# Optimization experiments

Measured on AMD Instinct MI355X. Metric: run time of the kernel, lower is better.

Reference implementation:

```python
import jax, jax.numpy as jnp
import numpy as np

NF, B, C, H, W = 5, 8, 64, 128, 128

def setup_inputs() -> dict:
    key = jax.random.key(0)
    k1, k2, k3, k4, k5 = jax.random.split(key, 5)
    return {
        "inp": jax.random.normal(k1, (NF, B, C, H, W), dtype=jnp.float32),
        "origin_w": jax.random.normal(k2, (C, NF * C), dtype=jnp.float32) * 0.05,
        "origin_b": jax.random.normal(k3, (C,), dtype=jnp.float32) * 0.05,
        "out_w": jax.random.normal(k4, (1, 2 * C), dtype=jnp.float32) * 0.05,
        "out_b": jax.random.normal(k5, (1,), dtype=jnp.float32) * 0.05,
    }

def reference(inp, origin_w, origin_b, out_w, out_b):
    nf, b, c, h, w = inp.shape
    # concat frames along channel dim: [b, nf*c, h, w]
    x = jnp.transpose(inp, (1, 0, 2, 3, 4)).reshape(b, nf * c, h, w)
    # 1x1 conv -> origin query, viewed as [b, c, 1, h*w]
    origin = jnp.einsum('ok,bkhw->bohw', origin_w, x) + origin_b[None, :, None, None]
    origin = origin.reshape(b, c, 1, h * w)
    last = inp[-1]  # [b, c, h, w]
    # difference basis: [b, c, nf-1, h*w]
    basis = jnp.stack([last - inp[i] for i in range(nf - 1)], axis=2).reshape(b, c, nf - 1, h * w)
    # L2 normalize over the spatial (last) dim, torch F.normalize semantics (eps=1e-12)
    norm = jnp.sqrt(jnp.sum(basis * basis, axis=-1, keepdims=True))
    basis1 = basis / jnp.maximum(norm, 1e-12)
    # tiny-MN batched matmuls: [b,c,1,hw] x [b,c,hw,nf-1] -> [b,c,1,nf-1]
    score = jnp.einsum('bcik,bcjk->bcij', origin, basis1)
    # [b,c,1,nf-1] x [b,c,nf-1,hw] -> [b,c,1,hw]; original views back as (b,c,w,h)
    out = jnp.einsum('bcij,bcjk->bcik', score, basis1).reshape(b, c, w, h)
    cat = jnp.concatenate([out, last], axis=1)  # [b, 2c, h, w]
    y = jnp.einsum('ok,bkhw->bohw', out_w, cat) + out_b[None, :, None, None]
    return y
```

## Files before the change

kernel.cpp:

```cpp
#include <hip/hip_runtime.h>
#include <math.h>

#define NF 5
#define NB 8
#define NC 64
#define HW 16384
#define NK 320
#define FSTRIDE (NB*NC*HW)

#define EN_FLOATS    (NB*NC*8)
#define ALPHA_FLOATS (NB*NK)

__global__ void k0_wp(const float* __restrict__ W, float* __restrict__ Wp){
    int idx = blockIdx.x*256 + threadIdx.x;
    if (idx < NC*NK){
        int c = idx / NK;
        int k = idx - c*NK;
        Wp[((c>>3)*NK + k)*8 + (c&7)] = W[idx];
    }
}

__device__ __forceinline__ float redsum64(float v){
#pragma unroll
    for (int m = 1; m < 64; m <<= 1) v += __shfl_xor(v, m, 64);
    return v;
}

__global__ __launch_bounds__(512, 4) void k1_fused(
    const float* __restrict__ inp, const float* __restrict__ Wp,
    const float* __restrict__ bias, float* __restrict__ EN)
{
    const int tid = threadIdx.x;
    const int l   = tid & 63;
    const int wv  = __builtin_amdgcn_readfirstlane(tid >> 6);
    const int c0  = wv << 3;
    const int b   = blockIdx.x >> 6;
    const int s0  = (blockIdx.x & 63) << 8;

    float4 a0,a1,a2,a3,a4,a5,a6,a7;
    {
        float4 b0 = *reinterpret_cast<const float4*>(bias + c0);
        float4 b1 = *reinterpret_cast<const float4*>(bias + c0 + 4);
        a0 = make_float4(b0.x,b0.x,b0.x,b0.x);
        a1 = make_float4(b0.y,b0.y,b0.y,b0.y);
        a2 = make_float4(b0.z,b0.z,b0.z,b0.z);
        a3 = make_float4(b0.w,b0.w,b0.w,b0.w);
        a4 = make_float4(b1.x,b1.x,b1.x,b1.x);
        a5 = make_float4(b1.y,b1.y,b1.y,b1.y);
        a6 = make_float4(b1.z,b1.z,b1.z,b1.z);
        a7 = make_float4(b1.w,b1.w,b1.w,b1.w);
    }

    const float* wbase = Wp + (size_t)wv * (NK*8);

#define FMA4(A, WS) \
    A.x = fmaf(WS, xv.x, A.x); A.y = fmaf(WS, xv.y, A.y); \
    A.z = fmaf(WS, xv.z, A.z); A.w = fmaf(WS, xv.w, A.w);

#pragma unroll 1
    for (int f=0; f<NF; ++f){
        const float* xp = inp + (size_t)(f*NB + b)*NC*HW + s0 + (l << 2);
        const float* wf = wbase + f*64*8;
#pragma unroll 8
        for (int k=0; k<64; ++k){
            float4 xv = *reinterpret_cast<const float4*>(xp);
            xp += HW;
            const float* wk = wf + (k << 3);
            float4 w0 = *reinterpret_cast<const float4*>(wk);
            float4 w1 = *reinterpret_cast<const float4*>(wk + 4);
            FMA4(a0, w0.x) FMA4(a1, w0.y) FMA4(a2, w0.z) FMA4(a3, w0.w)
            FMA4(a4, w1.x) FMA4(a5, w1.y) FMA4(a6, w1.z) FMA4(a7, w1.w)
        }
    }
#undef FMA4

#define PHASEB(CC, ACC) { \
    const float* cb = inp + ((size_t)b*NC + (c0+(CC)))*HW + s0 + (l << 2); \
    float4 x4 = *reinterpret_cast<const float4*>(cb + (size_t)4*FSTRIDE); \
    float ev[4], nv[4]; \
    _Pragma("unroll") \
    for (int i=0; i<4; ++i){ \
        float4 xi = *reinterpret_cast<const float4*>(cb + (size_t)i*FSTRIDE); \
        float dx = x4.x - xi.x, dy = x4.y - xi.y; \
        float dz = x4.z - xi.z, dw = x4.w - xi.w; \
        nv[i] = fmaf(dx,dx, fmaf(dy,dy, fmaf(dz,dz, dw*dw))); \
        ev[i] = fmaf((ACC).x,dx, fmaf((ACC).y,dy, fmaf((ACC).z,dz, (ACC).w*dw))); \
    } \
    _Pragma("unroll") \
    for (int i=0; i<4; ++i){ ev[i] = redsum64(ev[i]); nv[i] = redsum64(nv[i]); } \
    if (l == 0){ \
        float* p = EN + ((size_t)b*NC + c0 + (CC))*8; \
        atomicAdd(p+0, ev[0]); atomicAdd(p+1, ev[1]); \
        atomicAdd(p+2, ev[2]); atomicAdd(p+3, ev[3]); \
        atomicAdd(p+4, nv[0]); atomicAdd(p+5, nv[1]); \
        atomicAdd(p+6, nv[2]); atomicAdd(p+7, nv[3]); \
    } }

    PHASEB(0, a0) PHASEB(1, a1) PHASEB(2, a2) PHASEB(3, a3)
    PHASEB(4, a4) PHASEB(5, a5) PHASEB(6, a6) PHASEB(7, a7)
#undef PHASEB
}

__global__ void k2_coef(const float* __restrict__ EN, const float* __restrict__ out_w,
                        float* __restrict__ alpha)
{
    int tid = threadIdx.x;
    int b = tid >> 6, c = tid & 63;
    const float* e = EN + (b*NC + c)*8;
    float w1 = out_w[c], w2 = out_w[NC + c];
    float csum = 0.f;
#pragma unroll
    for (int i=0; i<4; ++i){
        float nc = fmaxf(sqrtf(e[4+i]), 1e-12f);
        float coef = e[i] / (nc*nc);
        alpha[b*NK + i*NC + c] = -w1*coef;
        csum += coef;
    }
    alpha[b*NK + 4*NC + c] = w1*csum + w2;
}

__global__ __launch_bounds__(512, 4) void k3_out(const float* __restrict__ inp,
        const float* __restrict__ alpha, const float* __restrict__ out_b,
        float* __restrict__ y)
{
    __shared__ float4 P[512];
    const int tid = threadIdx.x;
    const int b   = blockIdx.x >> 6;
    const int s0  = (blockIdx.x & 63) << 8;
    const int sg  = tid & 63;
    const int rg  = __builtin_amdgcn_readfirstlane(tid >> 6);

    float4 acc = make_float4(0.f, 0.f, 0.f, 0.f);
    const float* abase = alpha + b*NK + rg*40;
#pragma unroll 8
    for (int j=0; j<40; ++j){
        int r = rg*40 + j;
        const float* p = inp + (size_t)(((r>>6)*NB + b)*NC + (r&63))*HW + s0 + (sg<<2);
        float  w  = abase[j];
        float4 xv = *reinterpret_cast<const float4*>(p);
        acc.x = fmaf(w, xv.x, acc.x); acc.y = fmaf(w, xv.y, acc.y);
        acc.z = fmaf(w, xv.z, acc.z); acc.w = fmaf(w, xv.w, acc.w);
    }
    P[tid] = acc;
    __syncthreads();
    if (tid < 64){
        float4 r0 = P[tid];
        float vx = r0.x, vy = r0.y, vz = r0.z, vw = r0.w;
#pragma unroll
        for (int g=1; g<8; ++g){
            float4 q = P[tid + (g<<6)];
            vx += q.x; vy += q.y; vz += q.z; vw += q.w;
        }
        float bb = out_b[0];
        float4 o = make_float4(vx+bb, vy+bb, vz+bb, vw+bb);
        *reinterpret_cast<float4*>(y + (size_t)b*HW + s0 + (tid<<2)) = o;
    }
}

extern "C" void kernel_launch(void* const* d_in, const int* in_sizes, int n_in,
                              void* d_out, int out_size, void* d_ws, size_t ws_size,
                              hipStream_t stream)
{
    const float* inp      = (const float*)d_in[0];
    const float* origin_w = (const float*)d_in[1];
    const float* origin_b = (const float*)d_in[2];
    const float* out_w    = (const float*)d_in[3];
    const float* out_b    = (const float*)d_in[4];
    float* y  = (float*)d_out;
    float* ws = (float*)d_ws;

    float* EN    = ws;
    float* alpha = ws + EN_FLOATS;
    float* Wp    = ws + EN_FLOATS + ALPHA_FLOATS;

    hipMemsetAsync(EN, 0, EN_FLOATS*sizeof(float), stream);
    k0_wp   <<<(NC*NK + 255)/256, 256, 0, stream>>>(origin_w, Wp);
    k1_fused<<<512, 512, 0, stream>>>(inp, Wp, origin_b, EN);
    k2_coef <<<1, NB*NC, 0, stream>>>(EN, out_w, alpha);
    k3_out  <<<512, 512, 0, stream>>>(inp, alpha, out_b, y);
}
```

Baseline: 330.0 us.

## Split k1 into 4-channel waves with XCD-aware mapping and fold coef kernel into k3

Reworks k1 so that each wave accumulates 4 output channels instead of 8, with 2048 blocks of 256 threads. Block indices are remapped so that the four channel-group blocks sharing a spatial tile land on the same XCD, which lets them share the input reads in L2. The memset is merged into the weight-repack kernel and the k2 coefficient kernel is folded into k3 through shared memory, removing two launches. The cost is that each input element is now read by four blocks instead of one, which leans on L2 hits, and k3 recomputes the coefficients in every block.

After: 353.5 us. +7.1%, slower.

```diff
diff --git a/kernel.cpp b/kernel.cpp
--- a/kernel.cpp
+++ b/kernel.cpp
@@ -9,15 +9,21 @@
 #define FSTRIDE (NB*NC*HW)
 
 #define EN_FLOATS    (NB*NC*8)
-#define ALPHA_FLOATS (NB*NK)
 
-__global__ void k0_wp(const float* __restrict__ W, float* __restrict__ Wp){
-    int idx = blockIdx.x*256 + threadIdx.x;
-    if (idx < NC*NK){
-        int c = idx / NK;
-        int k = idx - c*NK;
-        Wp[((c>>3)*NK + k)*8 + (c&7)] = W[idx];
+__global__ void k0_wp(const float* __restrict__ W, float* __restrict__ Wp,
+                      float* __restrict__ EN){
+    const int blk = blockIdx.x, tid = threadIdx.x;
+    if (blk == 80){
+        float4 z = make_float4(0.f,0.f,0.f,0.f);
+#pragma unroll
+        for (int j=0; j<4; ++j)
+            reinterpret_cast<float4*>(EN)[tid*4 + j] = z;
+        return;
     }
+    int idx = blk*256 + tid;
+    int c = idx / NK;
+    int k = idx - c*NK;
+    Wp[((c>>2)*NK + k)*4 + (c&3)] = W[idx];
 }
 
 __device__ __forceinline__ float redsum64(float v){
@@ -26,32 +32,33 @@
     return v;
 }
 
-__global__ __launch_bounds__(512, 4) void k1_fused(
+__global__ __launch_bounds__(256, 8) void k1_fused(
     const float* __restrict__ inp, const float* __restrict__ Wp,
     const float* __restrict__ bias, float* __restrict__ EN)
 {
     const int tid = threadIdx.x;
     const int l   = tid & 63;
     const int wv  = __builtin_amdgcn_readfirstlane(tid >> 6);
-    const int c0  = wv << 3;
-    const int b   = blockIdx.x >> 6;
-    const int s0  = (blockIdx.x & 63) << 8;
+    const int blk = blockIdx.x;
+    const int xcd  = blk & 7;
+    const int slot = blk >> 3;
+    const int cgrp = slot & 3;
+    const int g    = xcd*64 + (slot >> 2);
+    const int b    = g >> 6;
+    const int s0   = (g & 63) << 8;
+    const int c0   = (cgrp << 4) + (wv << 2);
+    const int sl   = __builtin_amdgcn_readfirstlane(c0 >> 2);
 
-    float4 a0,a1,a2,a3,a4,a5,a6,a7;
+    float4 a0,a1,a2,a3;
     {
-        float4 b0 = *reinterpret_cast<const float4*>(bias + c0);
-        float4 b1 = *reinterpret_cast<const float4*>(bias + c0 + 4);
-        a0 = make_float4(b0.x,b0.x,b0.x,b0.x);
-        a1 = make_float4(b0.y,b0.y,b0.y,b0.y);
-        a2 = make_float4(b0.z,b0.z,b0.z,b0.z);
-        a3 = make_float4(b0.w,b0.w,b0.w,b0.w);
-        a4 = make_float4(b1.x,b1.x,b1.x,b1.x);
-        a5 = make_float4(b1.y,b1.y,b1.y,b1.y);
-        a6 = make_float4(b1.z,b1.z,b1.z,b1.z);
-        a7 = make_float4(b1.w,b1.w,b1.w,b1.w);
+        float4 bv = *reinterpret_cast<const float4*>(bias + c0);
+        a0 = make_float4(bv.x,bv.x,bv.x,bv.x);
+        a1 = make_float4(bv.y,bv.y,bv.y,bv.y);
+        a2 = make_float4(bv.z,bv.z,bv.z,bv.z);
+        a3 = make_float4(bv.w,bv.w,bv.w,bv.w);
     }
 
-    const float* wbase = Wp + (size_t)wv * (NK*8);
+    const float* wsl = Wp + (size_t)sl * (NK*4);
 
 #define FMA4(A, WS) \
     A.x = fmaf(WS, xv.x, A.x); A.y = fmaf(WS, xv.y, A.y); \
@@ -60,16 +67,13 @@
 #pragma unroll 1
     for (int f=0; f<NF; ++f){
         const float* xp = inp + (size_t)(f*NB + b)*NC*HW + s0 + (l << 2);
-        const float* wf = wbase + f*64*8;
+        const float* wf = wsl + f*256;
 #pragma unroll 8
         for (int k=0; k<64; ++k){
             float4 xv = *reinterpret_cast<const float4*>(xp);
             xp += HW;
-            const float* wk = wf + (k << 3);
-            float4 w0 = *reinterpret_cast<const float4*>(wk);
-            float4 w1 = *reinterpret_cast<const float4*>(wk + 4);
-            FMA4(a0, w0.x) FMA4(a1, w0.y) FMA4(a2, w0.z) FMA4(a3, w0.w)
-            FMA4(a4, w1.x) FMA4(a5, w1.y) FMA4(a6, w1.z) FMA4(a7, w1.w)
+            float4 w  = *reinterpret_cast<const float4*>(wf + (k << 2));
+            FMA4(a0, w.x) FMA4(a1, w.y) FMA4(a2, w.z) FMA4(a3, w.w)
         }
     }
 #undef FMA4
@@ -97,32 +101,14 @@
     } }
 
     PHASEB(0, a0) PHASEB(1, a1) PHASEB(2, a2) PHASEB(3, a3)
-    PHASEB(4, a4) PHASEB(5, a5) PHASEB(6, a6) PHASEB(7, a7)
 #undef PHASEB
 }
 
-__global__ void k2_coef(const float* __restrict__ EN, const float* __restrict__ out_w,
-                        float* __restrict__ alpha)
+__global__ __launch_bounds__(512) void k3_out(const float* __restrict__ inp,
+        const float* __restrict__ EN, const float* __restrict__ out_w,
+        const float* __restrict__ out_b, float* __restrict__ y)
 {
-    int tid = threadIdx.x;
-    int b = tid >> 6, c = tid & 63;
-    const float* e = EN + (b*NC + c)*8;
-    float w1 = out_w[c], w2 = out_w[NC + c];
-    float csum = 0.f;
-#pragma unroll
-    for (int i=0; i<4; ++i){
-        float nc = fmaxf(sqrtf(e[4+i]), 1e-12f);
-        float coef = e[i] / (nc*nc);
-        alpha[b*NK + i*NC + c] = -w1*coef;
-        csum += coef;
-    }
-    alpha[b*NK + 4*NC + c] = w1*csum + w2;
-}
-
-__global__ __launch_bounds__(512, 4) void k3_out(const float* __restrict__ inp,
-        const float* __restrict__ alpha, const float* __restrict__ out_b,
-        float* __restrict__ y)
-{
+    __shared__ float  Al[NK];
     __shared__ float4 P[512];
     const int tid = threadIdx.x;
     const int b   = blockIdx.x >> 6;
@@ -130,13 +116,29 @@
     const int sg  = tid & 63;
     const int rg  = __builtin_amdgcn_readfirstlane(tid >> 6);
 
+    if (tid < 64){
+        const int c = tid;
+        const float* e = EN + ((size_t)b*NC + c)*8;
+        float w1 = out_w[c], w2 = out_w[NC + c];
+        float csum = 0.f;
+#pragma unroll
+        for (int i=0; i<4; ++i){
+            float nc = fmaxf(sqrtf(e[4+i]), 1e-12f);
+            float coef = e[i] / (nc*nc);
+            Al[i*NC + c] = -w1*coef;
+            csum += coef;
+        }
+        Al[4*NC + c] = w1*csum + w2;
+    }
+    __syncthreads();
+
     float4 acc = make_float4(0.f, 0.f, 0.f, 0.f);
-    const float* abase = alpha + b*NK + rg*40;
+    const int rbase = rg*40;
 #pragma unroll 8
     for (int j=0; j<40; ++j){
-        int r = rg*40 + j;
+        int r = rbase + j;
         const float* p = inp + (size_t)(((r>>6)*NB + b)*NC + (r&63))*HW + s0 + (sg<<2);
-        float  w  = abase[j];
+        float  w  = Al[r];
         float4 xv = *reinterpret_cast<const float4*>(p);
         acc.x = fmaf(w, xv.x, acc.x); acc.y = fmaf(w, xv.y, acc.y);
         acc.z = fmaf(w, xv.z, acc.z); acc.w = fmaf(w, xv.w, acc.w);
@@ -147,8 +149,8 @@
         float4 r0 = P[tid];
         float vx = r0.x, vy = r0.y, vz = r0.z, vw = r0.w;
 #pragma unroll
-        for (int g=1; g<8; ++g){
-            float4 q = P[tid + (g<<6)];
+        for (int gg=1; gg<8; ++gg){
+            float4 q = P[tid + (gg<<6)];
             vx += q.x; vy += q.y; vz += q.z; vw += q.w;
         }
         float bb = out_b[0];
@@ -169,13 +171,10 @@
     float* y  = (float*)d_out;
     float* ws = (float*)d_ws;
 
-    float* EN    = ws;
-    float* alpha = ws + EN_FLOATS;
-    float* Wp    = ws + EN_FLOATS + ALPHA_FLOATS;
+    float* EN = ws;
+    float* Wp = ws + EN_FLOATS;
 
-    hipMemsetAsync(EN, 0, EN_FLOATS*sizeof(float), stream);
-    k0_wp   <<<(NC*NK + 255)/256, 256, 0, stream>>>(origin_w, Wp);
-    k1_fused<<<512, 512, 0, stream>>>(inp, Wp, origin_b, EN);
-    k2_coef <<<1, NB*NC, 0, stream>>>(EN, out_w, alpha);
-    k3_out  <<<512, 512, 0, stream>>>(inp, alpha, out_b, y);
+    k0_wp   <<<81,   256, 0, stream>>>(origin_w, Wp, EN);
+    k1_fused<<<2048, 256, 0, stream>>>(inp, Wp, origin_b, EN);
+    k3_out  <<<512,  512, 0, stream>>>(inp, EN, out_w, out_b, y);
 }
```
